# Kernel tuning notes

Measured on AMD Instinct MI355X. Metric: run time of the kernel, lower is better.

The kernel has to match this reference:

```python
import jax, jax.numpy as jnp
import numpy as np

B, T, D, H = 2, 2048, 1024, 16
HD = D // H  # head_dim = 64

def setup_inputs() -> dict:
    key = jax.random.key(0)
    ks = jax.random.split(key, 5)
    s = 0.02
    return {
        "x": jax.random.normal(ks[0], (B, T, D), dtype=jnp.float32),
        "w_qkv": jax.random.normal(ks[1], (3 * D, D), dtype=jnp.float32) * s,
        "b_qkv": jax.random.normal(ks[2], (3 * D,), dtype=jnp.float32) * s,
        "w_proj": jax.random.normal(ks[3], (D, D), dtype=jnp.float32) * s,
        "b_proj": jax.random.normal(ks[4], (D,), dtype=jnp.float32) * s,
    }

def reference(x, w_qkv, b_qkv, w_proj, b_proj):
    b, t, c = x.shape
    h, hd = H, HD
    scale = hd ** -0.5
    # qkv projection (torch Linear: x @ W^T + b)
    qkv = x @ w_qkv.T + b_qkv                      # [b, t, 3c]
    q, k, v = jnp.split(qkv, 3, axis=-1)
    # b t (h d) -> b h t d
    reshape = lambda z: z.reshape(b, t, h, hd).transpose(0, 2, 1, 3)
    q, k, v = reshape(q), reshape(k), reshape(v)
    scores = jnp.einsum("bhqd,bhkd->bhqk", q, k) * scale  # [b, h, t, t]
    causal = jnp.triu(jnp.ones((t, t), dtype=bool), k=1)   # True above diag
    scores = jnp.where(causal[None, None], -jnp.inf, scores)
    attn = jax.nn.softmax(scores, axis=-1)
    out = jnp.einsum("bhqk,bhkd->bhqd", attn, v)            # [b, h, t, d]
    out = out.transpose(0, 2, 1, 3).reshape(b, t, c)        # b h t d -> b t (h d)
    return out @ w_proj.T + b_proj
```

## Files before the change

kernel.cpp:

```cpp
#include <hip/hip_runtime.h>
#include <hip/hip_bf16.h>

#define Bq 2
#define Tq 2048
#define Dq 1024
#define Hq 16
#define HDq 64

typedef __attribute__((ext_vector_type(8))) short short8;
typedef __attribute__((ext_vector_type(4))) float f32x4;

__device__ __forceinline__ unsigned short f2bf(float f) {
  union { float f; unsigned int i; } v; v.f = f;
  unsigned int r = v.i + 0x7fffu + ((v.i >> 16) & 1u);
  return (unsigned short)(r >> 16);
}
__device__ __forceinline__ unsigned short f2bf_fast(float f) {
  union { float f; unsigned int i; } v; v.f = f;
  return (unsigned short)((v.i + 0x8000u) >> 16);
}

__device__ __forceinline__ short8 cvt8(const float* __restrict__ g) {
  const float4* gp = (const float4*)g;
  float4 x0 = gp[0], x1 = gp[1];
  short8 v;
  v[0] = (short)f2bf(x0.x); v[1] = (short)f2bf(x0.y);
  v[2] = (short)f2bf(x0.z); v[3] = (short)f2bf(x0.w);
  v[4] = (short)f2bf(x1.x); v[5] = (short)f2bf(x1.y);
  v[6] = (short)f2bf(x1.z); v[7] = (short)f2bf(x1.w);
  return v;
}

__device__ __forceinline__ void async_cp16(const void* g, void* l) {
  __builtin_amdgcn_global_load_lds(
      (const __attribute__((address_space(1))) void*)g,
      (__attribute__((address_space(3))) void*)l, 16, 0, 0);
}

constexpr int NXC = (Bq * Tq * Dq) / 8;
constexpr int NW1C = (3 * Dq * Dq) / 8;
constexpr int NW2C = (Dq * Dq) / 8;

__global__ __launch_bounds__(256)
void cvt_all(const float* __restrict__ x, const float* __restrict__ w1,
             const float* __restrict__ w2, unsigned short* __restrict__ xo,
             unsigned short* __restrict__ w1o, unsigned short* __restrict__ w2o)
{
  int i = blockIdx.x * 256 + threadIdx.x;
  const float* src; unsigned short* dst; int j;
  if (i < NXC)              { src = x;  dst = xo;  j = i; }
  else if (i < NXC + NW1C)  { src = w1; dst = w1o; j = i - NXC; }
  else                      { src = w2; dst = w2o; j = i - NXC - NW1C; }
  *(short8*)&dst[(size_t)j * 8] = cvt8(src + (size_t)j * 8);
}

template<int EPI, int BN_>
__global__ __launch_bounds__(256)
void gemm_bt(const unsigned short* __restrict__ Ab, const unsigned short* __restrict__ Wb,
             const float* __restrict__ bias, float* __restrict__ outp,
             int K, int N,
             unsigned short* __restrict__ qo, unsigned short* __restrict__ ko,
             unsigned short* __restrict__ vo)
{
  constexpr int WN = BN_ / 2;
  constexpr int NJ = WN / 16;
  constexpr int NBI = BN_ / 64;
  __shared__ unsigned short As[128 * 32];
  __shared__ unsigned short Bs[BN_ * 32];

  const int t = threadIdx.x;
  const int lane = t & 63, w = t >> 6;
  const int m0 = blockIdx.y * 128, n0 = blockIdx.x * BN_;
  const int fr = lane & 15, qd = lane >> 4;
  const int wm = (w >> 1) * 64, wn = (w & 1) * WN;

  f32x4 acc[4][NJ] = {};

  for (int k0 = 0; k0 < K; k0 += 32) {
    __syncthreads();
    #pragma unroll
    for (int j = 0; j < 2; j++) {
      int G = (2 * w + j) * 64 + lane;
      int row = G >> 2, g = G & 3;
      async_cp16(Ab + (size_t)(m0 + row) * K + k0 + g * 8, &As[G * 8]);
    }
    #pragma unroll
    for (int j = 0; j < NBI; j++) {
      int G = (NBI * w + j) * 64 + lane;
      int row = G >> 2, g = G & 3;
      async_cp16(Wb + (size_t)(n0 + row) * K + k0 + g * 8, &Bs[G * 8]);
    }
    __syncthreads();
    short8 af[4], bf[NJ];
    #pragma unroll
    for (int ib = 0; ib < 4; ib++)
      af[ib] = *(const short8*)&As[(wm + ib * 16 + fr) * 32 + qd * 8];
    #pragma unroll
    for (int jb = 0; jb < NJ; jb++)
      bf[jb] = *(const short8*)&Bs[(wn + jb * 16 + fr) * 32 + qd * 8];
    #pragma unroll
    for (int ib = 0; ib < 4; ib++)
      #pragma unroll
      for (int jb = 0; jb < NJ; jb++)
        acc[ib][jb] = __builtin_amdgcn_mfma_f32_16x16x32_bf16(af[ib], bf[jb], acc[ib][jb], 0, 0, 0);
  }

  #pragma unroll
  for (int jb = 0; jb < NJ; jb++) {
    int col = n0 + wn + jb * 16 + fr;
    float bv = bias[col];
    if (EPI == 0) {
      int which = col >> 10;
      int rem = col & 1023;
      int hh = rem >> 6, dd = rem & 63;
      #pragma unroll
      for (int ib = 0; ib < 4; ib++) {
        int row4 = m0 + wm + ib * 16 + qd * 4;
        int bb = row4 >> 11, tt = row4 & (Tq - 1);
        if (which == 2) {
          unsigned lo = (unsigned)f2bf(acc[ib][jb][0] + bv)
                      | ((unsigned)f2bf(acc[ib][jb][1] + bv) << 16);
          unsigned hi = (unsigned)f2bf(acc[ib][jb][2] + bv)
                      | ((unsigned)f2bf(acc[ib][jb][3] + bv) << 16);
          uint2 pk; pk.x = lo; pk.y = hi;
          *(uint2*)&vo[((size_t)(bb * Hq + hh) * HDq + dd) * Tq + tt] = pk;
        } else {
          unsigned short* dst = (which == 0) ? qo : ko;
          #pragma unroll
          for (int r = 0; r < 4; r++)
            dst[((size_t)(bb * Hq + hh) * Tq + tt + r) * HDq + dd] = f2bf(acc[ib][jb][r] + bv);
        }
      }
    } else {
      #pragma unroll
      for (int ib = 0; ib < 4; ib++)
        #pragma unroll
        for (int r = 0; r < 4; r++) {
          int row = m0 + wm + ib * 16 + qd * 4 + r;
          outp[(size_t)row * N + col] = acc[ib][jb][r] + bv;
        }
    }
  }
}

constexpr int AP = 72;

template<bool DIAG>
__device__ __forceinline__ void strip_compute(
    const short8 aq0, const short8 aq1,
    const short8 (&bk)[4][2], const short8 (&bv)[4][2], const short8 ones,
    unsigned short* __restrict__ PsRow, int fr, int qd, int qbase,
    f32x4 (&oacc)[4], f32x4& lacc, float SCL)
{
  f32x4 s4[4] = {};
  #pragma unroll
  for (int nb = 0; nb < 4; nb++) {
    s4[nb] = __builtin_amdgcn_mfma_f32_16x16x32_bf16(aq0, bk[nb][0], s4[nb], 0, 0, 0);
    s4[nb] = __builtin_amdgcn_mfma_f32_16x16x32_bf16(aq1, bk[nb][1], s4[nb], 0, 0, 0);
  }
  #pragma unroll
  for (int nb = 0; nb < 4; nb++)
    #pragma unroll
    for (int reg = 0; reg < 4; reg++) {
      float pv = exp2f(s4[nb][reg] * SCL);
      if (DIAG && (nb * 16 + fr) > (qbase + reg)) pv = 0.f;
      PsRow[(qd * 4 + reg) * AP + nb * 16 + fr] = f2bf_fast(pv);
    }
  short8 ap0 = *(const short8*)&PsRow[fr * AP + qd * 8];
  short8 ap1 = *(const short8*)&PsRow[fr * AP + 32 + qd * 8];
  lacc = __builtin_amdgcn_mfma_f32_16x16x32_bf16(ap0, ones, lacc, 0, 0, 0);
  lacc = __builtin_amdgcn_mfma_f32_16x16x32_bf16(ap1, ones, lacc, 0, 0, 0);
  #pragma unroll
  for (int db = 0; db < 4; db++) {
    oacc[db] = __builtin_amdgcn_mfma_f32_16x16x32_bf16(ap0, bv[db][0], oacc[db], 0, 0, 0);
    oacc[db] = __builtin_amdgcn_mfma_f32_16x16x32_bf16(ap1, bv[db][1], oacc[db], 0, 0, 0);
  }
}

__global__ __launch_bounds__(256, 2)
void attn_fwd(const unsigned short* __restrict__ qb, const unsigned short* __restrict__ kb,
              const unsigned short* __restrict__ vtb, unsigned short* __restrict__ ab)
{
  __shared__ unsigned short Ks[2][64 * 64];
  __shared__ unsigned short Vts[2][64 * 64];
  __shared__ unsigned short Ps[128 * AP];

  const int t = threadIdx.x, w = t >> 6, lane = t & 63;
  const int fr = lane & 15, qd = lane >> 4;
  const int p = blockIdx.x;
  const int bh = blockIdx.y;
  const int sB = 31 - p;
  const int sA = p;
  const int s0t[2] = { sB * 64, sA * 64 };
  const int ktB = sB;
  const int qbase = w * 16 + qd * 4;

  short8 aq[2][2];
  #pragma unroll
  for (int tl = 0; tl < 2; tl++) {
    const unsigned short* Qg = qb + ((size_t)bh * Tq + s0t[tl]) * HDq;
    #pragma unroll
    for (int c = 0; c < 2; c++)
      aq[tl][c] = *(const short8*)(Qg + (w * 16 + fr) * 64 + c * 32 + qd * 8);
  }

  const unsigned short* Kbh = kb + (size_t)bh * Tq * HDq;
  const unsigned short* Vbh = vtb + (size_t)bh * HDq * Tq;

  const int off0 = ((qd ^ (fr & 7)) * 8);
  const int off1 = off0 ^ 32;

  const int G0 = 2 * w * 64 + lane, G1 = G0 + 64;
  const int r0 = G0 >> 3, g0 = (G0 & 7) ^ (r0 & 7);
  const int r1 = G1 >> 3, g1 = (G1 & 7) ^ (r1 & 7);

  short8 ones;
  #pragma unroll
  for (int j = 0; j < 8; j++) ones[j] = (short)0x3F80;

  f32x4 oacc[2][4] = {};
  f32x4 lacc[2] = {};
  const float SCL = 0.125f * 1.44269504088896f;

  unsigned short* PsB = &Ps[(0 * 64 + w * 16) * AP];
  unsigned short* PsA = &Ps[(1 * 64 + w * 16) * AP];

  async_cp16(Kbh + (size_t)r0 * 64 + g0 * 8, &Ks[0][G0 * 8]);
  async_cp16(Vbh + (size_t)r0 * Tq + g0 * 8, &Vts[0][G0 * 8]);
  async_cp16(Kbh + (size_t)r1 * 64 + g1 * 8, &Ks[0][G1 * 8]);
  async_cp16(Vbh + (size_t)r1 * Tq + g1 * 8, &Vts[0][G1 * 8]);

  for (int kt = 0; kt <= ktB; kt++) {
    const int cur = kt & 1;
    __syncthreads();
    if (kt < ktB) {
      const int nxt = cur ^ 1;
      const size_t kofs = (size_t)(kt + 1) * 64;
      async_cp16(Kbh + (kofs + r0) * 64 + g0 * 8, &Ks[nxt][G0 * 8]);
      async_cp16(Vbh + (size_t)r0 * Tq + kofs + g0 * 8, &Vts[nxt][G0 * 8]);
      async_cp16(Kbh + (kofs + r1) * 64 + g1 * 8, &Ks[nxt][G1 * 8]);
      async_cp16(Vbh + (size_t)r1 * Tq + kofs + g1 * 8, &Vts[nxt][G1 * 8]);
    }

    short8 bk[4][2], bv[4][2];
    #pragma unroll
    for (int nb = 0; nb < 4; nb++) {
      bk[nb][0] = *(const short8*)&Ks[cur][(nb * 16 + fr) * 64 + off0];
      bk[nb][1] = *(const short8*)&Ks[cur][(nb * 16 + fr) * 64 + off1];
      bv[nb][0] = *(const short8*)&Vts[cur][(nb * 16 + fr) * 64 + off0];
      bv[nb][1] = *(const short8*)&Vts[cur][(nb * 16 + fr) * 64 + off1];
    }

    if (kt == ktB)
      strip_compute<true >(aq[0][0], aq[0][1], bk, bv, ones, PsB, fr, qd, qbase, oacc[0], lacc[0], SCL);
    else
      strip_compute<false>(aq[0][0], aq[0][1], bk, bv, ones, PsB, fr, qd, qbase, oacc[0], lacc[0], SCL);

    if (kt < sA)
      strip_compute<false>(aq[1][0], aq[1][1], bk, bv, ones, PsA, fr, qd, qbase, oacc[1], lacc[1], SCL);
    else if (kt == sA)
      strip_compute<true >(aq[1][0], aq[1][1], bk, bv, ones, PsA, fr, qd, qbase, oacc[1], lacc[1], SCL);
  }

  #pragma unroll
  for (int tl = 0; tl < 2; tl++)
    #pragma unroll
    for (int reg = 0; reg < 4; reg++) {
      float linv = 1.0f / lacc[tl][reg];
      size_t rowoff = ((size_t)(bh >> 4) * Tq + s0t[tl] + w * 16 + qd * 4 + reg) * Dq
                    + (bh & 15) * HDq;
      #pragma unroll
      for (int db = 0; db < 4; db++)
        ab[rowoff + db * 16 + fr] = f2bf(oacc[tl][db][reg] * linv);
    }
}

extern "C" void kernel_launch(void* const* d_in, const int* in_sizes, int n_in,
                              void* d_out, int out_size, void* d_ws, size_t ws_size,
                              hipStream_t stream) {
  const float* x      = (const float*)d_in[0];
  const float* w_qkv  = (const float*)d_in[1];
  const float* b_qkv  = (const float*)d_in[2];
  const float* w_proj = (const float*)d_in[3];
  const float* b_proj = (const float*)d_in[4];
  float* out = (float*)d_out;

  unsigned short* ws = (unsigned short*)d_ws;
  const size_t NE = (size_t)Bq * Hq * Tq * HDq;
  unsigned short* qb  = ws;
  unsigned short* kb  = ws + NE;
  unsigned short* vtb = ws + 2 * NE;
  unsigned short* ab  = ws + 3 * NE;
  unsigned short* xb  = ws + 4 * NE;
  unsigned short* wqb = xb + (size_t)NXC * 8;
  unsigned short* wpb = wqb + (size_t)NW1C * 8;

  dim3 blk(256);
  cvt_all<<<dim3((NXC + NW1C + NW2C) >> 8), blk, 0, stream>>>(x, w_qkv, w_proj, xb, wqb, wpb);

  dim3 g1(3 * Dq / 128, Bq * Tq / 128);
  gemm_bt<0, 128><<<g1, blk, 0, stream>>>(xb, wqb, b_qkv, nullptr,
                                          Dq, 3 * Dq, qb, kb, vtb);
  dim3 g2(16, Bq * Hq);
  attn_fwd<<<g2, blk, 0, stream>>>(qb, kb, vtb, ab);
  dim3 g3(Dq / 64, Bq * Tq / 128);
  gemm_bt<1, 64><<<g3, blk, 0, stream>>>(ab, wpb, b_proj, out,
                                         Dq, Dq, nullptr, nullptr, nullptr);
}
```

Baseline: 197.8 us.

## Split paired attention strips into one strip per block and deepen GEMM K-step

The attention kernel stops pairing a long and a short causal query strip in one block. It now launches one block per 64-row strip, doubling the grid, halving the P shared buffer and raising the occupancy hint to 3. The GEMM loads a 64-wide K slab per iteration as two 32-wide panels, halving the number of barriers per K loop. The trade-off is that the balanced pairing is lost, so per-block work becomes uneven, which relies on the hardware scheduler to balance load. The larger GEMM shared-memory tiles may also reduce occupancy.

```diff
diff --git a/kernel.cpp b/kernel.cpp
--- a/kernel.cpp
+++ b/kernel.cpp
@@ -64,9 +64,10 @@
 {
   constexpr int WN = BN_ / 2;
   constexpr int NJ = WN / 16;
-  constexpr int NBI = BN_ / 64;
-  __shared__ unsigned short As[128 * 32];
-  __shared__ unsigned short Bs[BN_ * 32];
+  constexpr int NAI = 4;
+  constexpr int NBI = BN_ / 32;
+  __shared__ unsigned short As[2 * 128 * 32];
+  __shared__ unsigned short Bs[2 * BN_ * 32];
 
   const int t = threadIdx.x;
   const int lane = t & 63, w = t >> 6;
@@ -76,33 +77,38 @@
 
   f32x4 acc[4][NJ] = {};
 
-  for (int k0 = 0; k0 < K; k0 += 32) {
+  for (int k0 = 0; k0 < K; k0 += 64) {
     __syncthreads();
     #pragma unroll
-    for (int j = 0; j < 2; j++) {
-      int G = (2 * w + j) * 64 + lane;
-      int row = G >> 2, g = G & 3;
-      async_cp16(Ab + (size_t)(m0 + row) * K + k0 + g * 8, &As[G * 8]);
+    for (int j = 0; j < NAI; j++) {
+      int G = j * 256 + t;
+      int panel = G >> 9, rowg = (G >> 2) & 127, colg = G & 3;
+      async_cp16(Ab + (size_t)(m0 + rowg) * K + k0 + panel * 32 + colg * 8, &As[G * 8]);
     }
     #pragma unroll
     for (int j = 0; j < NBI; j++) {
-      int G = (NBI * w + j) * 64 + lane;
-      int row = G >> 2, g = G & 3;
-      async_cp16(Wb + (size_t)(n0 + row) * K + k0 + g * 8, &Bs[G * 8]);
+      int G = j * 256 + t;
+      int panel = G >> 9, rowg = (G >> 2) & (BN_ - 1), colg = G & 3;
+      if (BN_ == 64) { panel = G >> 8 >> 1; rowg = (G >> 2) & 63; }
+      panel = G / (BN_ * 4); rowg = (G / 4) % BN_; colg = G & 3;
+      async_cp16(Wb + (size_t)(n0 + rowg) * K + k0 + panel * 32 + colg * 8, &Bs[G * 8]);
     }
     __syncthreads();
-    short8 af[4], bf[NJ];
-    #pragma unroll
-    for (int ib = 0; ib < 4; ib++)
-      af[ib] = *(const short8*)&As[(wm + ib * 16 + fr) * 32 + qd * 8];
-    #pragma unroll
-    for (int jb = 0; jb < NJ; jb++)
-      bf[jb] = *(const short8*)&Bs[(wn + jb * 16 + fr) * 32 + qd * 8];
-    #pragma unroll
-    for (int ib = 0; ib < 4; ib++)
+    #pragma unroll
+    for (int kh = 0; kh < 2; kh++) {
+      short8 af[4], bf[NJ];
+      #pragma unroll
+      for (int ib = 0; ib < 4; ib++)
+        af[ib] = *(const short8*)&As[kh * 4096 + (wm + ib * 16 + fr) * 32 + qd * 8];
       #pragma unroll
       for (int jb = 0; jb < NJ; jb++)
-        acc[ib][jb] = __builtin_amdgcn_mfma_f32_16x16x32_bf16(af[ib], bf[jb], acc[ib][jb], 0, 0, 0);
+        bf[jb] = *(const short8*)&Bs[kh * (BN_ * 32) + (wn + jb * 16 + fr) * 32 + qd * 8];
+      #pragma unroll
+      for (int ib = 0; ib < 4; ib++)
+        #pragma unroll
+        for (int jb = 0; jb < NJ; jb++)
+          acc[ib][jb] = __builtin_amdgcn_mfma_f32_16x16x32_bf16(af[ib], bf[jb], acc[ib][jb], 0, 0, 0);
+    }
   }
 
   #pragma unroll
@@ -177,32 +183,24 @@
   }
 }
 
-__global__ __launch_bounds__(256, 2)
+__global__ __launch_bounds__(256, 3)
 void attn_fwd(const unsigned short* __restrict__ qb, const unsigned short* __restrict__ kb,
               const unsigned short* __restrict__ vtb, unsigned short* __restrict__ ab)
 {
   __shared__ unsigned short Ks[2][64 * 64];
   __shared__ unsigned short Vts[2][64 * 64];
-  __shared__ unsigned short Ps[128 * AP];
+  __shared__ unsigned short Ps[64 * AP];
 
   const int t = threadIdx.x, w = t >> 6, lane = t & 63;
   const int fr = lane & 15, qd = lane >> 4;
-  const int p = blockIdx.x;
+  const int s = 31 - (int)blockIdx.x;
   const int bh = blockIdx.y;
-  const int sB = 31 - p;
-  const int sA = p;
-  const int s0t[2] = { sB * 64, sA * 64 };
-  const int ktB = sB;
+  const int q0 = s * 64;
   const int qbase = w * 16 + qd * 4;
 
-  short8 aq[2][2];
-  #pragma unroll
-  for (int tl = 0; tl < 2; tl++) {
-    const unsigned short* Qg = qb + ((size_t)bh * Tq + s0t[tl]) * HDq;
-    #pragma unroll
-    for (int c = 0; c < 2; c++)
-      aq[tl][c] = *(const short8*)(Qg + (w * 16 + fr) * 64 + c * 32 + qd * 8);
-  }
+  const unsigned short* Qg = qb + ((size_t)bh * Tq + q0) * HDq;
+  const short8 aq0 = *(const short8*)(Qg + (w * 16 + fr) * 64 + qd * 8);
+  const short8 aq1 = *(const short8*)(Qg + (w * 16 + fr) * 64 + 32 + qd * 8);
 
   const unsigned short* Kbh = kb + (size_t)bh * Tq * HDq;
   const unsigned short* Vbh = vtb + (size_t)bh * HDq * Tq;
@@ -218,22 +216,21 @@
   #pragma unroll
   for (int j = 0; j < 8; j++) ones[j] = (short)0x3F80;
 
-  f32x4 oacc[2][4] = {};
-  f32x4 lacc[2] = {};
+  f32x4 oacc[4] = {};
+  f32x4 lacc = {};
   const float SCL = 0.125f * 1.44269504088896f;
 
-  unsigned short* PsB = &Ps[(0 * 64 + w * 16) * AP];
-  unsigned short* PsA = &Ps[(1 * 64 + w * 16) * AP];
+  unsigned short* PsRow = &Ps[(w * 16) * AP];
 
   async_cp16(Kbh + (size_t)r0 * 64 + g0 * 8, &Ks[0][G0 * 8]);
   async_cp16(Vbh + (size_t)r0 * Tq + g0 * 8, &Vts[0][G0 * 8]);
   async_cp16(Kbh + (size_t)r1 * 64 + g1 * 8, &Ks[0][G1 * 8]);
   async_cp16(Vbh + (size_t)r1 * Tq + g1 * 8, &Vts[0][G1 * 8]);
 
-  for (int kt = 0; kt <= ktB; kt++) {
+  for (int kt = 0; kt <= s; kt++) {
     const int cur = kt & 1;
     __syncthreads();
-    if (kt < ktB) {
+    if (kt < s) {
       const int nxt = cur ^ 1;
       const size_t kofs = (size_t)(kt + 1) * 64;
       async_cp16(Kbh + (kofs + r0) * 64 + g0 * 8, &Ks[nxt][G0 * 8]);
@@ -251,28 +248,21 @@
       bv[nb][1] = *(const short8*)&Vts[cur][(nb * 16 + fr) * 64 + off1];
     }
 
-    if (kt == ktB)
-      strip_compute<true >(aq[0][0], aq[0][1], bk, bv, ones, PsB, fr, qd, qbase, oacc[0], lacc[0], SCL);
+    if (kt == s)
+      strip_compute<true >(aq0, aq1, bk, bv, ones, PsRow, fr, qd, qbase, oacc, lacc, SCL);
     else
-      strip_compute<false>(aq[0][0], aq[0][1], bk, bv, ones, PsB, fr, qd, qbase, oacc[0], lacc[0], SCL);
-
-    if (kt < sA)
-      strip_compute<false>(aq[1][0], aq[1][1], bk, bv, ones, PsA, fr, qd, qbase, oacc[1], lacc[1], SCL);
-    else if (kt == sA)
-      strip_compute<true >(aq[1][0], aq[1][1], bk, bv, ones, PsA, fr, qd, qbase, oacc[1], lacc[1], SCL);
-  }
-
-  #pragma unroll
-  for (int tl = 0; tl < 2; tl++)
-    #pragma unroll
-    for (int reg = 0; reg < 4; reg++) {
-      float linv = 1.0f / lacc[tl][reg];
-      size_t rowoff = ((size_t)(bh >> 4) * Tq + s0t[tl] + w * 16 + qd * 4 + reg) * Dq
-                    + (bh & 15) * HDq;
-      #pragma unroll
-      for (int db = 0; db < 4; db++)
-        ab[rowoff + db * 16 + fr] = f2bf(oacc[tl][db][reg] * linv);
-    }
+      strip_compute<false>(aq0, aq1, bk, bv, ones, PsRow, fr, qd, qbase, oacc, lacc, SCL);
+  }
+
+  #pragma unroll
+  for (int reg = 0; reg < 4; reg++) {
+    float linv = 1.0f / lacc[reg];
+    size_t rowoff = ((size_t)(bh >> 4) * Tq + q0 + w * 16 + qd * 4 + reg) * Dq
+                  + (bh & 15) * HDq;
+    #pragma unroll
+    for (int db = 0; db < 4; db++)
+      ab[rowoff + db * 16 + fr] = f2bf(oacc[db][reg] * linv);
+  }
 }
 
 extern "C" void kernel_launch(void* const* d_in, const int* in_sizes, int n_in,
@@ -301,7 +291,7 @@
   dim3 g1(3 * Dq / 128, Bq * Tq / 128);
   gemm_bt<0, 128><<<g1, blk, 0, stream>>>(xb, wqb, b_qkv, nullptr,
                                           Dq, 3 * Dq, qb, kb, vtb);
-  dim3 g2(16, Bq * Hq);
+  dim3 g2(32, Bq * Hq);
   attn_fwd<<<g2, blk, 0, stream>>>(qb, kb, vtb, ab);
   dim3 g3(Dq / 64, Bq * Tq / 128);
   gemm_bt<1, 64><<<g3, blk, 0, stream>>>(ab, wpb, b_proj, out,
```

Result: slower. 222.5 us (+12.5%).

## Double-buffer GEMM K tiles and interleave paired attention strips

Applied to the files above, without the earlier changes.

The GEMM kernel now loads 64-wide K tiles into double-buffered shared memory, prefetching the next tile while computing the current one, which halves the number of barriers per K step. The attention kernel fuses the two query-strip computations into one routine that interleaves their MFMA chains, giving the scheduler independent work to hide MFMA latency. Shared memory use in the GEMM grows fourfold, which may lower occupancy. The dual path assumes strip B is never on its diagonal while kt <= sA, which holds because sB = 31 - p is greater than sA for the launched blocks.

```diff
diff --git a/kernel.cpp b/kernel.cpp
--- a/kernel.cpp
+++ b/kernel.cpp
@@ -64,9 +64,10 @@
 {
   constexpr int WN = BN_ / 2;
   constexpr int NJ = WN / 16;
-  constexpr int NBI = BN_ / 64;
-  __shared__ unsigned short As[128 * 32];
-  __shared__ unsigned short Bs[BN_ * 32];
+  constexpr int NAI = 4;
+  constexpr int NBI = BN_ / 32;
+  __shared__ unsigned short As[2][2 * 128 * 32];
+  __shared__ unsigned short Bs[2][2 * BN_ * 32];
 
   const int t = threadIdx.x;
   const int lane = t & 63, w = t >> 6;
@@ -75,34 +76,55 @@
   const int wm = (w >> 1) * 64, wn = (w & 1) * WN;
 
   f32x4 acc[4][NJ] = {};
-
-  for (int k0 = 0; k0 < K; k0 += 32) {
+  const int NIT = K / 64;
+
+  #pragma unroll
+  for (int j = 0; j < NAI; j++) {
+    int G = j * 256 + t;
+    int panel = G >> 9, rowg = (G >> 2) & 127, colg = G & 3;
+    async_cp16(Ab + (size_t)(m0 + rowg) * K + panel * 32 + colg * 8, &As[0][G * 8]);
+  }
+  #pragma unroll
+  for (int j = 0; j < NBI; j++) {
+    int G = j * 256 + t;
+    int panel = G / (BN_ * 4), rowg = (G / 4) % BN_, colg = G & 3;
+    async_cp16(Wb + (size_t)(n0 + rowg) * K + panel * 32 + colg * 8, &Bs[0][G * 8]);
+  }
+
+  for (int i = 0; i < NIT; i++) {
+    const int cur = i & 1;
     __syncthreads();
-    #pragma unroll
-    for (int j = 0; j < 2; j++) {
-      int G = (2 * w + j) * 64 + lane;
-      int row = G >> 2, g = G & 3;
-      async_cp16(Ab + (size_t)(m0 + row) * K + k0 + g * 8, &As[G * 8]);
-    }
-    #pragma unroll
-    for (int j = 0; j < NBI; j++) {
-      int G = (NBI * w + j) * 64 + lane;
-      int row = G >> 2, g = G & 3;
-      async_cp16(Wb + (size_t)(n0 + row) * K + k0 + g * 8, &Bs[G * 8]);
-    }
-    __syncthreads();
-    short8 af[4], bf[NJ];
-    #pragma unroll
-    for (int ib = 0; ib < 4; ib++)
-      af[ib] = *(const short8*)&As[(wm + ib * 16 + fr) * 32 + qd * 8];
-    #pragma unroll
-    for (int jb = 0; jb < NJ; jb++)
-      bf[jb] = *(const short8*)&Bs[(wn + jb * 16 + fr) * 32 + qd * 8];
-    #pragma unroll
-    for (int ib = 0; ib < 4; ib++)
+    if (i + 1 < NIT) {
+      const int nxt = cur ^ 1;
+      const int k0 = (i + 1) * 64;
+      #pragma unroll
+      for (int j = 0; j < NAI; j++) {
+        int G = j * 256 + t;
+        int panel = G >> 9, rowg = (G >> 2) & 127, colg = G & 3;
+        async_cp16(Ab + (size_t)(m0 + rowg) * K + k0 + panel * 32 + colg * 8, &As[nxt][G * 8]);
+      }
+      #pragma unroll
+      for (int j = 0; j < NBI; j++) {
+        int G = j * 256 + t;
+        int panel = G / (BN_ * 4), rowg = (G / 4) % BN_, colg = G & 3;
+        async_cp16(Wb + (size_t)(n0 + rowg) * K + k0 + panel * 32 + colg * 8, &Bs[nxt][G * 8]);
+      }
+    }
+    #pragma unroll
+    for (int kh = 0; kh < 2; kh++) {
+      short8 af[4], bf[NJ];
+      #pragma unroll
+      for (int ib = 0; ib < 4; ib++)
+        af[ib] = *(const short8*)&As[cur][kh * 4096 + (wm + ib * 16 + fr) * 32 + qd * 8];
       #pragma unroll
       for (int jb = 0; jb < NJ; jb++)
-        acc[ib][jb] = __builtin_amdgcn_mfma_f32_16x16x32_bf16(af[ib], bf[jb], acc[ib][jb], 0, 0, 0);
+        bf[jb] = *(const short8*)&Bs[cur][kh * (BN_ * 32) + (wn + jb * 16 + fr) * 32 + qd * 8];
+      #pragma unroll
+      for (int ib = 0; ib < 4; ib++)
+        #pragma unroll
+        for (int jb = 0; jb < NJ; jb++)
+          acc[ib][jb] = __builtin_amdgcn_mfma_f32_16x16x32_bf16(af[ib], bf[jb], acc[ib][jb], 0, 0, 0);
+    }
   }
 
   #pragma unroll
@@ -146,7 +168,7 @@
 constexpr int AP = 72;
 
 template<bool DIAG>
-__device__ __forceinline__ void strip_compute(
+__device__ __forceinline__ void strip_one(
     const short8 aq0, const short8 aq1,
     const short8 (&bk)[4][2], const short8 (&bv)[4][2], const short8 ones,
     unsigned short* __restrict__ PsRow, int fr, int qd, int qbase,
@@ -174,6 +196,55 @@
   for (int db = 0; db < 4; db++) {
     oacc[db] = __builtin_amdgcn_mfma_f32_16x16x32_bf16(ap0, bv[db][0], oacc[db], 0, 0, 0);
     oacc[db] = __builtin_amdgcn_mfma_f32_16x16x32_bf16(ap1, bv[db][1], oacc[db], 0, 0, 0);
+  }
+}
+
+template<bool SMALLDIAG>
+__device__ __forceinline__ void strip_dual(
+    const short8 (&aqB)[2], const short8 (&aqA)[2],
+    const short8 (&bk)[4][2], const short8 (&bv)[4][2], const short8 ones,
+    unsigned short* __restrict__ PsB, unsigned short* __restrict__ PsA,
+    int fr, int qd, int qbase,
+    f32x4 (&oB)[4], f32x4& lB, f32x4 (&oA)[4], f32x4& lA, float SCL)
+{
+  f32x4 sB[4] = {}, sA[4] = {};
+  #pragma unroll
+  for (int nb = 0; nb < 4; nb++) {
+    sB[nb] = __builtin_amdgcn_mfma_f32_16x16x32_bf16(aqB[0], bk[nb][0], sB[nb], 0, 0, 0);
+    sA[nb] = __builtin_amdgcn_mfma_f32_16x16x32_bf16(aqA[0], bk[nb][0], sA[nb], 0, 0, 0);
+  }
+  #pragma unroll
+  for (int nb = 0; nb < 4; nb++) {
+    sB[nb] = __builtin_amdgcn_mfma_f32_16x16x32_bf16(aqB[1], bk[nb][1], sB[nb], 0, 0, 0);
+    sA[nb] = __builtin_amdgcn_mfma_f32_16x16x32_bf16(aqA[1], bk[nb][1], sA[nb], 0, 0, 0);
+  }
+  #pragma unroll
+  for (int nb = 0; nb < 4; nb++)
+    #pragma unroll
+    for (int reg = 0; reg < 4; reg++) {
+      float pvB = exp2f(sB[nb][reg] * SCL);
+      float pvA = exp2f(sA[nb][reg] * SCL);
+      if (SMALLDIAG && (nb * 16 + fr) > (qbase + reg)) pvA = 0.f;
+      PsB[(qd * 4 + reg) * AP + nb * 16 + fr] = f2bf_fast(pvB);
+      PsA[(qd * 4 + reg) * AP + nb * 16 + fr] = f2bf_fast(pvA);
+    }
+  short8 apB0 = *(const short8*)&PsB[fr * AP + qd * 8];
+  short8 apB1 = *(const short8*)&PsB[fr * AP + 32 + qd * 8];
+  short8 apA0 = *(const short8*)&PsA[fr * AP + qd * 8];
+  short8 apA1 = *(const short8*)&PsA[fr * AP + 32 + qd * 8];
+  lB = __builtin_amdgcn_mfma_f32_16x16x32_bf16(apB0, ones, lB, 0, 0, 0);
+  lA = __builtin_amdgcn_mfma_f32_16x16x32_bf16(apA0, ones, lA, 0, 0, 0);
+  lB = __builtin_amdgcn_mfma_f32_16x16x32_bf16(apB1, ones, lB, 0, 0, 0);
+  lA = __builtin_amdgcn_mfma_f32_16x16x32_bf16(apA1, ones, lA, 0, 0, 0);
+  #pragma unroll
+  for (int db = 0; db < 4; db++) {
+    oB[db] = __builtin_amdgcn_mfma_f32_16x16x32_bf16(apB0, bv[db][0], oB[db], 0, 0, 0);
+    oA[db] = __builtin_amdgcn_mfma_f32_16x16x32_bf16(apA0, bv[db][0], oA[db], 0, 0, 0);
+  }
+  #pragma unroll
+  for (int db = 0; db < 4; db++) {
+    oB[db] = __builtin_amdgcn_mfma_f32_16x16x32_bf16(apB1, bv[db][1], oB[db], 0, 0, 0);
+    oA[db] = __builtin_amdgcn_mfma_f32_16x16x32_bf16(apA1, bv[db][1], oA[db], 0, 0, 0);
   }
 }
 
@@ -251,15 +322,19 @@
       bv[nb][1] = *(const short8*)&Vts[cur][(nb * 16 + fr) * 64 + off1];
     }
 
-    if (kt == ktB)
-      strip_compute<true >(aq[0][0], aq[0][1], bk, bv, ones, PsB, fr, qd, qbase, oacc[0], lacc[0], SCL);
-    else
-      strip_compute<false>(aq[0][0], aq[0][1], bk, bv, ones, PsB, fr, qd, qbase, oacc[0], lacc[0], SCL);
-
-    if (kt < sA)
-      strip_compute<false>(aq[1][0], aq[1][1], bk, bv, ones, PsA, fr, qd, qbase, oacc[1], lacc[1], SCL);
-    else if (kt == sA)
-      strip_compute<true >(aq[1][0], aq[1][1], bk, bv, ones, PsA, fr, qd, qbase, oacc[1], lacc[1], SCL);
+    if (kt < sA) {
+      strip_dual<false>(aq[0], aq[1], bk, bv, ones, PsB, PsA, fr, qd, qbase,
+                        oacc[0], lacc[0], oacc[1], lacc[1], SCL);
+    } else if (kt == sA) {
+      strip_dual<true >(aq[0], aq[1], bk, bv, ones, PsB, PsA, fr, qd, qbase,
+                        oacc[0], lacc[0], oacc[1], lacc[1], SCL);
+    } else if (kt == ktB) {
+      strip_one<true >(aq[0][0], aq[0][1], bk, bv, ones, PsB, fr, qd, qbase,
+                       oacc[0], lacc[0], SCL);
+    } else {
+      strip_one<false>(aq[0][0], aq[0][1], bk, bv, ones, PsB, fr, qd, qbase,
+                       oacc[0], lacc[0], SCL);
+    }
   }
 
   #pragma unroll
```

After: 198.3 us. No clear change (+0.2%).
